# Optimization experiments

Hardware: AMD Instinct MI355X
Metric: run time of the kernel (lower is better)

Reference implementation:

```python
import jax, jax.numpy as jnp
import numpy as np

NUM_EMB = 256
EMB_DIM = 32
B, N = 16, 16384
TEMPERATURE = 1.0      # current value of the temperature buffer
TEMP_MIN = 0.5
TEMP_INIT_REF = 2.0    # constant used in temp_ratio denominator in the torch code


def setup_inputs() -> dict:
    key = jax.random.key(0)
    k1, k2, k3 = jax.random.split(key, 3)
    inputs = jax.random.normal(k1, (B, N, EMB_DIM), dtype=jnp.float32)
    embedding = jax.random.normal(k2, (NUM_EMB, EMB_DIM), dtype=jnp.float32) * 0.1
    gumbel_u = jax.random.uniform(k3, (B * N, NUM_EMB), dtype=jnp.float32)
    return {"inputs": inputs, "embedding": embedding, "gumbel_u": gumbel_u}


def reference(inputs, embedding, gumbel_u):
    input_shape = inputs.shape
    flat = inputs.reshape(-1, EMB_DIM)                       # [M, D]

    distances = (jnp.sum(flat ** 2, axis=1, keepdims=True)
                 - 2.0 * jnp.matmul(flat, embedding.T)
                 + jnp.sum(embedding ** 2, axis=1))
    logits = -distances / TEMPERATURE

    # training branch: gumbel noise + softmax at temperature
    gumbel = -jnp.log(-jnp.log(gumbel_u + 1e-20) + 1e-20)
    soft = jax.nn.softmax((logits + gumbel) / TEMPERATURE, axis=-1)  # [M, K]

    quantized_soft = jnp.matmul(soft, embedding)             # [M, D]
    indices = jnp.argmax(soft, axis=-1)                      # [M]
    quantized_hard = embedding[indices]                      # [M, D]

    temp_ratio = (TEMPERATURE - TEMP_MIN) / (TEMP_INIT_REF - TEMP_MIN)
    quantized = temp_ratio * quantized_soft + (1.0 - temp_ratio) * quantized_hard
    # straight-through estimator
    quantized = flat + jax.lax.stop_gradient(quantized - flat)

    commitment_loss = jnp.mean((jax.lax.stop_gradient(quantized_hard) - flat) ** 2)

    avg_probs = jnp.mean(soft, axis=0)                       # [K]
    perplexity = jnp.exp(-jnp.sum(avg_probs * jnp.log(avg_probs + 1e-10)))

    quantized = quantized.reshape(input_shape)
    indices = indices.reshape(input_shape[:-1])
    return quantized, commitment_loss, indices, perplexity
```

## Files before the change

kernel.cpp:

```cpp
#include <hip/hip_runtime.h>


#define M_ROWS  262144
#define OUT_LOSS 8388608
#define OUT_IDX  8388609
#define OUT_PPL  8650753

#if defined(__has_builtin)
#if __has_builtin(__builtin_amdgcn_global_load_lds)
#define HAVE_GLLDS 1
#else
#define HAVE_GLLDS 0
#endif
#else
#define HAVE_GLLDS 0
#endif

typedef float f32x2 __attribute__((ext_vector_type(2)));

__device__ __forceinline__ f32x2 mk2(float a, float b) {
  f32x2 r; r.x = a; r.y = b; return r;
}

__device__ __forceinline__ unsigned int f2bf_u(float f) {
  unsigned int u = __float_as_uint(f);
  u += 0x7fffu + ((u >> 16) & 1u);
  return u >> 16;
}
__device__ __forceinline__ float bf2f(unsigned int lo16) {
  return __uint_as_float(lo16 << 16);
}

__global__ __launch_bounds__(256) void vq_prep(const float* __restrict__ emb,
                                               float* __restrict__ ws) {
  int t = threadIdx.x;
  ws[t] = 0.0f;
  if (t == 0) ws[256] = 0.0f;
  const float4* e4 = (const float4*)emb;
  float s = 0.0f;
#pragma unroll
  for (int j = 0; j < 8; ++j) {
    float4 v = e4[t * 8 + j];
    s += v.x * v.x + v.y * v.y + v.z * v.z + v.w * v.w;
  }
  ws[257 + t] = s;
}

__global__ __launch_bounds__(256, 4) void vq_pass1(
    const float* __restrict__ x_in, const float* __restrict__ emb,
    const float* __restrict__ gum, const float* __restrict__ ne,
    float* __restrict__ invS_ws, unsigned short* __restrict__ p_ws,
    float* __restrict__ loss_ws, float* __restrict__ out) {
  __shared__ __align__(16) float x_lds[16 * 36];
  __shared__ __align__(16) float g_lds[16 * 256];
  __shared__ float t_lds[256 * 17];
  __shared__ float red_sum[16 * 17];
  __shared__ float red_max[16 * 17];
  __shared__ int   red_idx[16 * 17];

  const int tid = threadIdx.x;
  const int wv  = tid >> 6;
  const int ln  = tid & 63;

  f32x2 er2[16];
  {
    const float4* e4 = (const float4*)(emb + tid * 32);
#pragma unroll
    for (int j = 0; j < 8; ++j) {
      float4 v = e4[j];
      er2[2*j]   = mk2(v.x, v.y);
      er2[2*j+1] = mk2(v.z, v.w);
    }
  }
  const float ne_t = ne[tid];
  const int row_blk = blockIdx.x * 256;
  float cl_acc = 0.0f;

#if HAVE_GLLDS
  auto issue_g = [&](int ttn) {
    const char* gbase = (const char*)(gum + (size_t)(row_blk + ttn * 16) * 256);
#pragma unroll
    for (int i = 0; i < 4; ++i) {
      const int off = i * 4096 + wv * 1024;
      __builtin_amdgcn_global_load_lds(
          (const __attribute__((address_space(1))) void*)(gbase + off + ln * 16),
          (__attribute__((address_space(3))) void*)((char*)g_lds + off),
          16, 0, 0);
    }
  };
  issue_g(0);
#endif

  for (int tt = 0; tt < 16; ++tt) {
    const int r0 = row_blk + tt * 16;

#if !HAVE_GLLDS
    {
      const float4* gg = (const float4*)gum + (size_t)r0 * 64;
      float4* gd = (float4*)g_lds;
#pragma unroll
      for (int i = 0; i < 4; ++i) gd[i * 256 + tid] = gg[i * 256 + tid];
    }
#endif
    if (tid < 128)
      *((float4*)&x_lds[(tid >> 3) * 36 + (tid & 7) * 4]) =
          ((const float4*)x_in)[(size_t)r0 * 8 + tid];
    __syncthreads();

#pragma unroll 2
    for (int r = 0; r < 16; ++r) {
      const float4* xr4 = (const float4*)&x_lds[r * 36];
      f32x2 a0 = mk2(0.f, 0.f), a1 = mk2(0.f, 0.f);
#pragma unroll
      for (int j = 0; j < 8; ++j) {
        const float4 xv = xr4[j];
        a0 = __builtin_elementwise_fma(mk2(xv.x, xv.y), er2[2*j],   a0);
        a1 = __builtin_elementwise_fma(mk2(xv.z, xv.w), er2[2*j+1], a1);
      }
      const float dot = (a0.x + a1.x) + (a0.y + a1.y);
      const float u = g_lds[r * 256 + tid];
      const float g = -__logf(-__logf(u + 1e-20f) + 1e-20f);
      t_lds[tid * 17 + r] = fmaf(2.0f, dot, g) - ne_t;
    }
    __syncthreads();

#if HAVE_GLLDS
    if (tt < 15) issue_g(tt + 1);
#endif

    const int lrow = tid & 15;
    const int cs   = tid >> 4;
    {
      float ssum = 0.0f, tmax = -3.0e38f;
      int   kmax = 0;
      unsigned int packs[8];
#pragma unroll
      for (int j = 0; j < 16; ++j) {
        const int k = cs * 16 + j;
        const float tv = t_lds[k * 17 + lrow];
        const float p = __expf(tv);
        ssum += p;
        if (tv > tmax) { tmax = tv; kmax = k; }
        if (j & 1) packs[j >> 1] |= f2bf_u(p) << 16;
        else       packs[j >> 1]  = f2bf_u(p);
      }
      uint4* pout = (uint4*)(p_ws + (size_t)(r0 + lrow) * 256 + cs * 16);
      const uint4* pd = (const uint4*)packs;
      pout[0] = pd[0]; pout[1] = pd[1];
      red_sum[lrow * 17 + cs] = ssum;
      red_max[lrow * 17 + cs] = tmax;
      red_idx[lrow * 17 + cs] = kmax;
    }
    __syncthreads();

    if (tid < 16) {
      float ssum = 0.0f, tmax = -3.0e38f;
      int   kmax = 0;
#pragma unroll
      for (int c = 0; c < 16; ++c) {
        ssum += red_sum[tid * 17 + c];
        const float m = red_max[tid * 17 + c];
        if (m > tmax) { tmax = m; kmax = red_idx[tid * 17 + c]; }
      }
      const int rg = r0 + tid;
      invS_ws[rg] = 1.0f / ssum;
      out[OUT_IDX + rg] = (float)kmax;

      const float4* eh = (const float4*)(emb + (size_t)kmax * 32);
      const float* xrr = &x_lds[tid * 36];
      float cl = 0.0f;
#pragma unroll
      for (int j = 0; j < 8; ++j) {
        const float4 e  = eh[j];
        const float4 xv = ((const float4*)xrr)[j];
        float dx;
        dx = e.x - xv.x; cl = fmaf(dx, dx, cl);
        dx = e.y - xv.y; cl = fmaf(dx, dx, cl);
        dx = e.z - xv.z; cl = fmaf(dx, dx, cl);
        dx = e.w - xv.w; cl = fmaf(dx, dx, cl);
      }
#pragma unroll
      for (int off = 8; off > 0; off >>= 1) cl += __shfl_down(cl, off, 16);
      if (tid == 0) cl_acc += cl;
    }
    __syncthreads();
  }
  if (tid == 0) atomicAdd(loss_ws, cl_acc);
}

__global__ __launch_bounds__(256, 4) void vq_pass2(
    const float* __restrict__ emb, const unsigned short* __restrict__ p_ws,
    const float* __restrict__ invS_ws, float* __restrict__ out) {
  __shared__ __align__(16) float e_lds[256 * 32];

  const int tid = threadIdx.x;
  {
    const float4* src = (const float4*)emb;
    float4* dst = (float4*)e_lds;
#pragma unroll
    for (int j = 0; j < 8; ++j) dst[j * 256 + tid] = src[j * 256 + tid];
  }
  __syncthreads();

  const int row = blockIdx.x * 256 + tid;
  const float invS = invS_ws[row];
  const int imax = (int)out[OUT_IDX + row];
  const uint4* pv = (const uint4*)(p_ws + (size_t)row * 256);
  const float4* el4 = (const float4*)e_lds;

  f32x2 q2[16];
#pragma unroll
  for (int d = 0; d < 16; ++d) q2[d] = mk2(0.f, 0.f);

  for (int kg = 0; kg < 8; ++kg) {
    unsigned int w_[16];
#pragma unroll
    for (int j = 0; j < 4; ++j) {
      const uint4 v = pv[kg * 4 + j];
      w_[4*j+0] = v.x; w_[4*j+1] = v.y; w_[4*j+2] = v.z; w_[4*j+3] = v.w;
    }
#pragma unroll
    for (int i = 0; i < 16; ++i) {
      const int k0 = kg * 32 + 2 * i;
      const f32x2 pp0 = mk2(bf2f(w_[i] & 0xffffu), bf2f(w_[i] & 0xffffu));
      const f32x2 pp1 = mk2(bf2f(w_[i] >> 16),     bf2f(w_[i] >> 16));
#pragma unroll
      for (int jj = 0; jj < 8; ++jj) {
        const float4 e0 = el4[k0 * 8 + jj];
        const float4 e1 = el4[(k0 + 1) * 8 + jj];
        q2[2*jj]   = __builtin_elementwise_fma(mk2(e0.x, e0.y), pp0, q2[2*jj]);
        q2[2*jj+1] = __builtin_elementwise_fma(mk2(e0.z, e0.w), pp0, q2[2*jj+1]);
        q2[2*jj]   = __builtin_elementwise_fma(mk2(e1.x, e1.y), pp1, q2[2*jj]);
        q2[2*jj+1] = __builtin_elementwise_fma(mk2(e1.z, e1.w), pp1, q2[2*jj+1]);
      }
    }
  }

  const float tr  = 1.0f / 3.0f;
  const float otr = 1.0f - tr;
  const float4* ehv = el4 + imax * 8;
  float4* outq = (float4*)(out + (size_t)row * 32);
#pragma unroll
  for (int j = 0; j < 8; ++j) {
    float4 e = ehv[j];
    float4 o;
    o.x = fmaf(tr, q2[2*j].x   * invS, otr * e.x);
    o.y = fmaf(tr, q2[2*j].y   * invS, otr * e.y);
    o.z = fmaf(tr, q2[2*j+1].x * invS, otr * e.z);
    o.w = fmaf(tr, q2[2*j+1].y * invS, otr * e.w);
    outq[j] = o;
  }
}

__global__ __launch_bounds__(256) void vq_avg(
    const unsigned short* __restrict__ p_ws, const float* __restrict__ invS_ws,
    float* __restrict__ avg_ws) {
  __shared__ float sh[256];
  const int tid = threadIdx.x, lane = tid & 63, w = tid >> 6;
  sh[tid] = 0.0f;
  __syncthreads();
  const int base = (blockIdx.x * 4 + w) * 32;
  const float iv = invS_ws[base + (lane & 31)];
  float a0 = 0.f, a1 = 0.f, a2 = 0.f, a3 = 0.f;
#pragma unroll 4
  for (int r = 0; r < 32; ++r) {
    const float s = __shfl(iv, r);
    const unsigned short* pr = p_ws + (size_t)(base + r) * 256;
    a0 = fmaf(bf2f(pr[  0 + lane]), s, a0);
    a1 = fmaf(bf2f(pr[ 64 + lane]), s, a1);
    a2 = fmaf(bf2f(pr[128 + lane]), s, a2);
    a3 = fmaf(bf2f(pr[192 + lane]), s, a3);
  }
  atomicAdd(&sh[  0 + lane], a0);
  atomicAdd(&sh[ 64 + lane], a1);
  atomicAdd(&sh[128 + lane], a2);
  atomicAdd(&sh[192 + lane], a3);
  __syncthreads();
  atomicAdd(&avg_ws[tid], sh[tid]);
}

__global__ __launch_bounds__(256) void vq_fin(const float* __restrict__ ws,
                                              float* __restrict__ out) {
  __shared__ float red[256];
  int t = threadIdx.x;
  float avg = ws[t] * (1.0f / 262144.0f);
  red[t] = -avg * __logf(avg + 1e-10f);
  __syncthreads();
  for (int s = 128; s > 0; s >>= 1) {
    if (t < s) red[t] += red[t + s];
    __syncthreads();
  }
  if (t == 0) {
    out[OUT_PPL]  = __expf(red[0]);
    out[OUT_LOSS] = ws[256] * (1.0f / 8388608.0f);
  }
}

__global__ __launch_bounds__(256, 1) void vq_main(
    const float* __restrict__ x_in, const float* __restrict__ emb,
    const float* __restrict__ gum, const float* __restrict__ ne,
    float* __restrict__ avg_ws, float* __restrict__ loss_ws,
    float* __restrict__ out) {
  extern __shared__ unsigned char dynsmem[];
  unsigned short* p_lds = (unsigned short*)dynsmem;

  const int tid  = threadIdx.x;
  const int lane = tid & 63;
  const int w    = tid >> 6;
  const int row  = blockIdx.x * 256 + tid;
  unsigned short* my_p = p_lds + (size_t)(w * 64 + lane) * 258;

  float xr[32];
  {
    const float4* xv = (const float4*)(x_in + (size_t)row * 32);
#pragma unroll
    for (int j = 0; j < 8; ++j) {
      float4 v = xv[j];
      xr[4*j+0] = v.x; xr[4*j+1] = v.y; xr[4*j+2] = v.z; xr[4*j+3] = v.w;
    }
  }
  float q[32];
#pragma unroll
  for (int d = 0; d < 32; ++d) q[d] = 0.0f;

  float ssum = 0.0f;
  float tmax = -3.0e38f;
  int   imax = 0;

  const float4* g4 = (const float4*)(gum + (size_t)row * 256);
  const float4* e4 = (const float4*)emb;

  for (int kg = 0; kg < 8; ++kg) {
    float uv[32];
#pragma unroll
    for (int j = 0; j < 8; ++j) {
      float4 v = g4[kg * 8 + j];
      uv[4*j+0] = v.x; uv[4*j+1] = v.y; uv[4*j+2] = v.z; uv[4*j+3] = v.w;
    }
#pragma unroll
    for (int kk = 0; kk < 32; ++kk) {
      const int k = kg * 32 + kk;
      float er[32];
#pragma unroll
      for (int j = 0; j < 8; ++j) {
        float4 v = e4[k * 8 + j];
        er[4*j+0] = v.x; er[4*j+1] = v.y; er[4*j+2] = v.z; er[4*j+3] = v.w;
      }
      float d0 = 0.f, d1 = 0.f, d2 = 0.f, d3 = 0.f;
#pragma unroll
      for (int d = 0; d < 32; d += 4) {
        d0 = fmaf(xr[d+0], er[d+0], d0);
        d1 = fmaf(xr[d+1], er[d+1], d1);
        d2 = fmaf(xr[d+2], er[d+2], d2);
        d3 = fmaf(xr[d+3], er[d+3], d3);
      }
      const float dot = (d0 + d1) + (d2 + d3);
      const float inner = -__logf(uv[kk] + 1e-20f);
      const float g = -__logf(inner + 1e-20f);
      const float t = fmaf(2.0f, dot, g) - ne[k];
      const float p = __expf(t);
      ssum += p;
      if (t > tmax) { tmax = t; imax = k; }
#pragma unroll
      for (int d = 0; d < 32; ++d) q[d] = fmaf(p, er[d], q[d]);
      my_p[k] = (unsigned short)f2bf_u(p);
    }
  }

  const float invS = 1.0f / ssum;
  {
    const float tr  = 1.0f / 3.0f;
    const float otr = 1.0f - tr;
    const float4* ehv = (const float4*)(emb + (size_t)imax * 32);
    float4* outq = (float4*)(out + (size_t)row * 32);
    float cl = 0.0f;
#pragma unroll
    for (int j = 0; j < 8; ++j) {
      float4 e = ehv[j];
      float4 o;
      float qs, dx;
      qs = q[4*j+0]*invS; o.x = tr*qs + otr*e.x; dx = e.x - xr[4*j+0]; cl = fmaf(dx,dx,cl);
      qs = q[4*j+1]*invS; o.y = tr*qs + otr*e.y; dx = e.y - xr[4*j+1]; cl = fmaf(dx,dx,cl);
      qs = q[4*j+2]*invS; o.z = tr*qs + otr*e.z; dx = e.z - xr[4*j+2]; cl = fmaf(dx,dx,cl);
      qs = q[4*j+3]*invS; o.w = tr*qs + otr*e.w; dx = e.w - xr[4*j+3]; cl = fmaf(dx,dx,cl);
      outq[j] = o;
    }
    out[OUT_IDX + row] = (float)imax;
#pragma unroll
    for (int off = 32; off > 0; off >>= 1) cl += __shfl_down(cl, off);
    if (lane == 0) atomicAdd(loss_ws, cl);
  }

  __syncthreads();

  float a0 = 0.f, a1 = 0.f, a2 = 0.f, a3 = 0.f;
  for (int r = 0; r < 64; ++r) {
    const float invS_r = __shfl(invS, r);
    const unsigned short* rp = p_lds + (size_t)(w * 64 + r) * 258;
    a0 = fmaf(bf2f(rp[  0 + lane]), invS_r, a0);
    a1 = fmaf(bf2f(rp[ 64 + lane]), invS_r, a1);
    a2 = fmaf(bf2f(rp[128 + lane]), invS_r, a2);
    a3 = fmaf(bf2f(rp[192 + lane]), invS_r, a3);
  }
  atomicAdd(&avg_ws[  0 + lane], a0);
  atomicAdd(&avg_ws[ 64 + lane], a1);
  atomicAdd(&avg_ws[128 + lane], a2);
  atomicAdd(&avg_ws[192 + lane], a3);
}

extern "C" void kernel_launch(void* const* d_in, const int* in_sizes, int n_in,
                              void* d_out, int out_size, void* d_ws, size_t ws_size,
                              hipStream_t stream) {
  const float* x   = (const float*)d_in[0];
  const float* emb = (const float*)d_in[1];
  const float* gum = (const float*)d_in[2];
  float* out = (float*)d_out;
  float* ws  = (float*)d_ws;

  (void)in_sizes; (void)n_in; (void)out_size;

  vq_prep<<<1, 256, 0, stream>>>(emb, ws);

  const size_t need = (size_t)(1024 + M_ROWS) * 4 + (size_t)M_ROWS * 256 * 2;
  if (ws_size >= need) {
    float* invS = ws + 1024;
    unsigned short* p = (unsigned short*)(ws + 1024 + M_ROWS);
    vq_pass1<<<1024, 256, 0, stream>>>(x, emb, gum, ws + 257, invS, p, ws + 256, out);
    vq_pass2<<<1024, 256, 0, stream>>>(emb, p, invS, out);
    vq_avg<<<2048, 256, 0, stream>>>(p, invS, ws);
  } else {
    hipFuncSetAttribute((const void*)vq_main,
                        hipFuncAttributeMaxDynamicSharedMemorySize, 132128);
    vq_main<<<1024, 256, 132128, stream>>>(x, emb, gum, ws + 257, ws, ws + 256, out);
  }
  vq_fin<<<1, 256, 0, stream>>>(ws, out);
}
```

Before: 319.0 us.

## Work in base-2 logits with prescaled codebook and widen vq_avg row loads

Pass1 now keeps logits in log2 space. The codebook registers are prescaled by 2*log2(e), the squared norms are computed locally times log2(e), and the Gumbel term is computed with log2 plus a constant offset, so the softmax uses exp2 directly instead of exp. This removes the separate norm buffer read and several multiplies from the inner loops. vq_avg now processes 64 rows per wave with 8-byte vector loads and launches half as many blocks, cutting atomic traffic and load instructions. The loop unroll is dropped to 1, and the base-2 rewrite changes rounding slightly.

```diff
diff --git a/kernel.cpp b/kernel.cpp
--- a/kernel.cpp
+++ b/kernel.cpp
@@ -48,7 +48,7 @@
 
 __global__ __launch_bounds__(256, 4) void vq_pass1(
     const float* __restrict__ x_in, const float* __restrict__ emb,
-    const float* __restrict__ gum, const float* __restrict__ ne,
+    const float* __restrict__ gum,
     float* __restrict__ invS_ws, unsigned short* __restrict__ p_ws,
     float* __restrict__ loss_ws, float* __restrict__ out) {
   __shared__ __align__(16) float x_lds[16 * 36];
@@ -62,17 +62,26 @@
   const int wv  = tid >> 6;
   const int ln  = tid & 63;
 
+  const float S2    = 2.8853900817779268f;
+  const float L2E   = 1.4426950408889634f;
+  const float GOFF  = 0.5287663729448977f;
+  const float EPS2  = 1.4426950408889634e-20f;
+
   f32x2 er2[16];
+  float ne_t;
   {
     const float4* e4 = (const float4*)(emb + tid * 32);
+    float na = 0.0f;
 #pragma unroll
     for (int j = 0; j < 8; ++j) {
       float4 v = e4[j];
-      er2[2*j]   = mk2(v.x, v.y);
-      er2[2*j+1] = mk2(v.z, v.w);
-    }
-  }
-  const float ne_t = ne[tid];
+      na = fmaf(v.x, v.x, na); na = fmaf(v.y, v.y, na);
+      na = fmaf(v.z, v.z, na); na = fmaf(v.w, v.w, na);
+      er2[2*j]   = mk2(v.x * S2, v.y * S2);
+      er2[2*j+1] = mk2(v.z * S2, v.w * S2);
+    }
+    ne_t = na * L2E;
+  }
   const int row_blk = blockIdx.x * 256;
   float cl_acc = 0.0f;
 
@@ -107,8 +116,11 @@
           ((const float4*)x_in)[(size_t)r0 * 8 + tid];
     __syncthreads();
 
-#pragma unroll 2
+#pragma unroll 1
     for (int r = 0; r < 16; ++r) {
+      const float u = g_lds[r * 256 + tid];
+      const float L1 = __log2f(u + 1e-20f);
+      const float gp = GOFF - __log2f(EPS2 - L1);
       const float4* xr4 = (const float4*)&x_lds[r * 36];
       f32x2 a0 = mk2(0.f, 0.f), a1 = mk2(0.f, 0.f);
 #pragma unroll
@@ -117,10 +129,8 @@
         a0 = __builtin_elementwise_fma(mk2(xv.x, xv.y), er2[2*j],   a0);
         a1 = __builtin_elementwise_fma(mk2(xv.z, xv.w), er2[2*j+1], a1);
       }
-      const float dot = (a0.x + a1.x) + (a0.y + a1.y);
-      const float u = g_lds[r * 256 + tid];
-      const float g = -__logf(-__logf(u + 1e-20f) + 1e-20f);
-      t_lds[tid * 17 + r] = fmaf(2.0f, dot, g) - ne_t;
+      const float dot2 = (a0.x + a1.x) + (a0.y + a1.y);
+      t_lds[tid * 17 + r] = dot2 + (gp - ne_t);
     }
     __syncthreads();
 
@@ -138,7 +148,7 @@
       for (int j = 0; j < 16; ++j) {
         const int k = cs * 16 + j;
         const float tv = t_lds[k * 17 + lrow];
-        const float p = __expf(tv);
+        const float p = exp2f(tv);
         ssum += p;
         if (tv > tmax) { tmax = tv; kmax = k; }
         if (j & 1) packs[j >> 1] |= f2bf_u(p) << 16;
@@ -259,22 +269,21 @@
   const int tid = threadIdx.x, lane = tid & 63, w = tid >> 6;
   sh[tid] = 0.0f;
   __syncthreads();
-  const int base = (blockIdx.x * 4 + w) * 32;
-  const float iv = invS_ws[base + (lane & 31)];
+  const int base = (blockIdx.x * 4 + w) * 64;
+  const float iv = invS_ws[base + lane];
   float a0 = 0.f, a1 = 0.f, a2 = 0.f, a3 = 0.f;
-#pragma unroll 4
-  for (int r = 0; r < 32; ++r) {
+  for (int r = 0; r < 64; ++r) {
     const float s = __shfl(iv, r);
-    const unsigned short* pr = p_ws + (size_t)(base + r) * 256;
-    a0 = fmaf(bf2f(pr[  0 + lane]), s, a0);
-    a1 = fmaf(bf2f(pr[ 64 + lane]), s, a1);
-    a2 = fmaf(bf2f(pr[128 + lane]), s, a2);
-    a3 = fmaf(bf2f(pr[192 + lane]), s, a3);
-  }
-  atomicAdd(&sh[  0 + lane], a0);
-  atomicAdd(&sh[ 64 + lane], a1);
-  atomicAdd(&sh[128 + lane], a2);
-  atomicAdd(&sh[192 + lane], a3);
+    const uint2 u2 = ((const uint2*)(p_ws + (size_t)(base + r) * 256))[lane];
+    a0 = fmaf(bf2f(u2.x & 0xffffu), s, a0);
+    a1 = fmaf(bf2f(u2.x >> 16),     s, a1);
+    a2 = fmaf(bf2f(u2.y & 0xffffu), s, a2);
+    a3 = fmaf(bf2f(u2.y >> 16),     s, a3);
+  }
+  atomicAdd(&sh[4*lane+0], a0);
+  atomicAdd(&sh[4*lane+1], a1);
+  atomicAdd(&sh[4*lane+2], a2);
+  atomicAdd(&sh[4*lane+3], a3);
   __syncthreads();
   atomicAdd(&avg_ws[tid], sh[tid]);
 }
@@ -425,11 +434,11 @@
   if (ws_size >= need) {
     float* invS = ws + 1024;
     unsigned short* p = (unsigned short*)(ws + 1024 + M_ROWS);
-    vq_pass1<<<1024, 256, 0, stream>>>(x, emb, gum, ws + 257, invS, p, ws + 256, out);
+    vq_pass1<<<1024, 256, 0, stream>>>(x, emb, gum, invS, p, ws + 256, out);
     vq_pass2<<<1024, 256, 0, stream>>>(emb, p, invS, out);
-    vq_avg<<<2048, 256, 0, stream>>>(p, invS, ws);
+    vq_avg<<<1024, 256, 0, stream>>>(p, invS, ws);
   } else {
-    hipFuncSetAttribute((const void*)vq_main,
+    (void)hipFuncSetAttribute((const void*)vq_main,
                         hipFuncAttributeMaxDynamicSharedMemorySize, 132128);
     vq_main<<<1024, 256, 132128, stream>>>(x, emb, gum, ws + 257, ws, ws + 256, out);
   }
```

Result: faster. 262.3 us (-17.8%).
